# Performance work log

Hardware: AMD Instinct MI355X
Metric: run time of the kernel (lower is better)

## Reference

```python
import jax, jax.numpy as jnp
import numpy as np

B, N, K, S_IN, S_OUT, C, FD = 32, 325, 20, 12, 12, 10, 64
ALPHA = 0.5  # LeakyReLU negative slope

def leaky(x):
    return jnp.where(x >= 0, x, ALPHA * x)

def setup_inputs() -> dict:
    key = jax.random.key(0)
    ks = jax.random.split(key, 9)
    s = 0.2
    return {
        "fushed_features": jax.random.normal(ks[0], (B, N, FD), jnp.float32),
        "input_data": jax.random.normal(ks[1], (B, N, S_IN), jnp.float32),
        "w_W": jax.random.normal(ks[2], (S_IN, S_OUT), jnp.float32) * s,
        "w_b": jax.random.normal(ks[3], (S_OUT,), jnp.float32) * s,
        "a1_W": jax.random.normal(ks[4], (2 * S_OUT, 4 * S_OUT), jnp.float32) * s,
        "a1_b": jax.random.normal(ks[5], (4 * S_OUT,), jnp.float32) * s,
        "a2_W": jax.random.normal(ks[6], (4 * S_OUT, C), jnp.float32) * s,
        "a2_b": jax.random.normal(ks[7], (C,), jnp.float32) * s,
        "adj_mx_topk_index": jax.random.randint(ks[8], (B, N, K), 0, N),
    }

def reference(fushed_features, input_data, w_W, w_b, a1_W, a1_b, a2_W, a2_b, adj_mx_topk_index):
    # w_net: Linear + LeakyReLU -> wh [B,N,S_OUT]
    wh = leaky(input_data @ w_W + w_b)
    # a_net on cat([wh_i, wh_j]): split first linear to avoid materializing [B,N,N,2*S_OUT]
    hx = wh @ a1_W[:S_OUT]   # contribution of wh_x (row node i)
    hy = wh @ a1_W[S_OUT:]   # contribution of wh_y (col node j)
    hidden = leaky(hx[:, :, None, :] + hy[:, None, :, :] + a1_b)   # [B,N,N,4*S_OUT]
    attention = leaky(hidden @ a2_W + a2_b)                        # [B,N,N,C]
    idx = adj_mx_topk_index                                        # [B,N,K]
    # gather top-k neighbors along dim 2
    idx_c = jnp.broadcast_to(idx[..., None], idx.shape + (attention.shape[-1],))
    attention_mask = jnp.take_along_axis(attention, idx_c, axis=2)  # [B,N,K,C]
    attention_mask = jax.nn.softmax(attention_mask, axis=-1)
    # gather neighbor features: wh_expand_top_k[b,i,k] = wh[b, idx[b,i,k]]
    wh_topk = wh[jnp.arange(wh.shape[0])[:, None, None], idx]       # [B,N,K,S_OUT]
    # output = attention_mask^T @ wh_topk
    output_data = jnp.einsum('bnkc,bnks->bncs', attention_mask, wh_topk)
    # clustering loss on detached neighbor features (cosine similarity)
    wt = jax.lax.stop_gradient(wh_topk)
    wtn = wt / (jnp.linalg.norm(wt, axis=-1, keepdims=True) + 1e-8)
    dist_mat = jnp.einsum('bnks,bnls->bnkl', wtn, wtn)              # [B,N,K,K]
    same = (dist_mat >= 0.5).astype(dist_mat.dtype)
    diff = 1.0 - same
    prob = jnp.einsum('bnkc,bnlc->bnkl', attention_mask, attention_mask)
    prob = jnp.clip(prob, 1e-4, 1.0 - 1e-4)
    logp = jnp.log(prob)
    cl = -(same * logp - diff * logp)
    cluster_loss = (cl.sum((-1, -2)) - jnp.trace(cl, axis1=-2, axis2=-1)).mean()
    return output_data, cluster_loss, dist_mat.mean(), wh.mean()
```

## Files before the change

kernel.cpp:

```cpp
#include <hip/hip_runtime.h>
#include <math.h>

#define Bdim 32
#define Ndim 325
#define Kdim 20
#define Sdim 12
#define Cdim 10
#define Hdim 48
#define NB   (Bdim*Ndim)
#define OUT_SCALARS (NB*Cdim*Sdim)
#define BN_BLOCKS (NB/4)
#define NODE_BLOCKS 260
#define NPB 40

#define O_WH  0
#define O_HX  (O_WH + NB*Sdim)
#define O_HY  (O_HX + NB*Hdim)
#define O_PCL (O_HY + NB*Hdim)
#define O_PDS (O_PCL + BN_BLOCKS)
#define O_PWH (O_PDS + BN_BLOCKS)
#define WS_BASE_FLOATS (O_PWH + NODE_BLOCKS)

__device__ __forceinline__ float leaky(float x) { return x >= 0.f ? x : 0.5f * x; }

__global__ __launch_bounds__(256)
void node_kernel(const float* __restrict__ x,
                 const float* __restrict__ wW, const float* __restrict__ wb,
                 const float* __restrict__ A1, const float* __restrict__ b1,
                 float* __restrict__ ws)
{
    __shared__ float s_wh[NPB][Sdim];
    __shared__ float s_r[4];
    const int tid = threadIdx.x;
    const int base = blockIdx.x * NPB;

    float v = 0.f;
    #pragma unroll
    for (int rep = 0; rep < 2; rep++) {
        const int e = tid + rep * 256;
        if (e < NPB * Sdim) {
            const int n = e / Sdim, s = e - n * Sdim;
            const float* xr = x + (size_t)(base + n) * Sdim;
            float acc = wb[s];
            #pragma unroll
            for (int i = 0; i < Sdim; i++) acc += xr[i] * wW[i * Sdim + s];
            acc = leaky(acc);
            s_wh[n][s] = acc;
            ws[O_WH + (size_t)(base + n) * Sdim + s] = acc;
            v += acc;
        }
    }
    __syncthreads();

    #pragma unroll
    for (int rep = 0; rep < 15; rep++) {
        const int e = tid + rep * 256;
        const int n = e / 96, r = e - n * 96;
        const int which = r / Hdim, d = r - which * Hdim;
        const float4 w0 = *(const float4*)&s_wh[n][0];
        const float4 w1 = *(const float4*)&s_wh[n][4];
        const float4 w2 = *(const float4*)&s_wh[n][8];
        const float* Ac = A1 + (which * Sdim) * Hdim + d;
        float acc = which ? 0.f : b1[d];
        acc += w0.x*Ac[0*Hdim] + w0.y*Ac[1*Hdim] + w0.z*Ac[2*Hdim] + w0.w*Ac[3*Hdim]
             + w1.x*Ac[4*Hdim] + w1.y*Ac[5*Hdim] + w1.z*Ac[6*Hdim] + w1.w*Ac[7*Hdim]
             + w2.x*Ac[8*Hdim] + w2.y*Ac[9*Hdim] + w2.z*Ac[10*Hdim] + w2.w*Ac[11*Hdim];
        ws[(which ? O_HY : O_HX) + (size_t)(base + n) * Hdim + d] = acc;
    }

    #pragma unroll
    for (int off = 32; off > 0; off >>= 1) v += __shfl_down(v, off);
    if ((tid & 63) == 0) s_r[tid >> 6] = v;
    __syncthreads();
    if (tid == 0) ws[O_PWH + blockIdx.x] = s_r[0] + s_r[1] + s_r[2] + s_r[3];
}

__device__ __forceinline__ float dot12(const float4& a0, const float4& a1, const float4& a2,
                                       const float4& b0, const float4& b1, const float4& b2)
{
    return a0.x*b0.x + a0.y*b0.y + a0.z*b0.z + a0.w*b0.w
         + a1.x*b1.x + a1.y*b1.y + a1.z*b1.z + a1.w*b1.w
         + a2.x*b2.x + a2.y*b2.y + a2.z*b2.z + a2.w*b2.w;
}

__global__ __launch_bounds__(256)
void mega_kernel(const int* __restrict__ topk,
                 const float* __restrict__ A2, const float* __restrict__ b2,
                 float* __restrict__ ws, float* __restrict__ out)
{
    __shared__ float s_A2  [Hdim * 12];
    __shared__ int   s_topk[80];
    __shared__ float s_whj [4][Kdim][12];
    __shared__ float s_am  [4][Kdim][12];
    __shared__ float s_invn[4][Kdim];
    __shared__ float s_red[2][4];

    const int tid = threadIdx.x;
    const int slot = tid >> 6, t = tid & 63;

    if (tid < 120) {
        const int e0 = tid * 4;
        #pragma unroll
        for (int u = 0; u < 4; u++) {
            const int e = e0 + u;
            const int d = e / Cdim, c = e - d * Cdim;
            s_A2[d * 12 + c] = A2[e];
        }
    } else if (tid < 200) {
        s_topk[tid - 120] = topk[blockIdx.x * 80 + (tid - 120)];
    }
    __syncthreads();

    if (tid < 160) {
        const int e = tid >> 1, half = tid & 1;
        const int gid = blockIdx.x * 80 + e;
        const int bn_e = gid / Kdim;
        const int b_e  = bn_e / Ndim;
        const int j    = s_topk[e];
        const int ek   = e / 20, kk = e - ek * 20;

        const float4* hx4 = (const float4*)(ws + O_HX + (size_t)bn_e * Hdim) + half * 6;
        const float4* hy4 = (const float4*)(ws + O_HY + ((size_t)b_e * Ndim + j) * Hdim) + half * 6;

        float4 xv[6], yv[6];
        #pragma unroll
        for (int q = 0; q < 6; q++) xv[q] = hx4[q];
        #pragma unroll
        for (int q = 0; q < 6; q++) yv[q] = hy4[q];

        float acc[Cdim];
        #pragma unroll
        for (int c = 0; c < Cdim; c++) acc[c] = 0.f;
        #pragma unroll
        for (int q = 0; q < 6; q++) {
            const float hh[4] = { leaky(xv[q].x + yv[q].x), leaky(xv[q].y + yv[q].y),
                                  leaky(xv[q].z + yv[q].z), leaky(xv[q].w + yv[q].w) };
            #pragma unroll
            for (int i = 0; i < 4; i++) {
                const int d = half * 24 + q * 4 + i;
                const float* Ar = &s_A2[d * 12];
                const float4 r0 = *(const float4*)(Ar + 0);
                const float4 r1 = *(const float4*)(Ar + 4);
                const float2 r2 = *(const float2*)(Ar + 8);
                const float h = hh[i];
                acc[0] += h * r0.x; acc[1] += h * r0.y;
                acc[2] += h * r0.z; acc[3] += h * r0.w;
                acc[4] += h * r1.x; acc[5] += h * r1.y;
                acc[6] += h * r1.z; acc[7] += h * r1.w;
                acc[8] += h * r2.x; acc[9] += h * r2.y;
            }
        }
        float full[Cdim];
        #pragma unroll
        for (int c = 0; c < Cdim; c++) full[c] = acc[c] + __shfl_xor(acc[c], 1);
        if (half == 0) {
            float m = -1e30f;
            #pragma unroll
            for (int c = 0; c < Cdim; c++) { full[c] = leaky(full[c] + b2[c]); m = fmaxf(m, full[c]); }
            float sum = 0.f;
            #pragma unroll
            for (int c = 0; c < Cdim; c++) { full[c] = __expf(full[c] - m); sum += full[c]; }
            const float inv = 1.f / sum;
            *(float4*)&s_am[ek][kk][0] = make_float4(full[0]*inv, full[1]*inv, full[2]*inv, full[3]*inv);
            *(float4*)&s_am[ek][kk][4] = make_float4(full[4]*inv, full[5]*inv, full[6]*inv, full[7]*inv);
            *(float4*)&s_am[ek][kk][8] = make_float4(full[8]*inv, full[9]*inv, 0.f, 0.f);
        }
    } else {
        for (int i = tid - 160; i < 240; i += 96) {
            const int kf = i / 3, q = i - kf * 3;
            const int sl = kf / 20, k = kf - sl * 20;
            const int bn_i = (blockIdx.x * 80 + kf) / Kdim;
            const int b_i  = bn_i / Ndim;
            const int j    = s_topk[kf];
            const float4 v = *(const float4*)(ws + O_WH + ((size_t)b_i * Ndim + j) * Sdim + q * 4);
            *(float4*)&s_whj[sl][k][q * 4] = v;
        }
    }
    __syncthreads();

    const int bn = blockIdx.x * 4 + slot;
    float cl = 0.f, ds = 0.f;

    if (t < Kdim) {
        const float4 w0 = *(const float4*)&s_whj[slot][t][0];
        const float4 w1 = *(const float4*)&s_whj[slot][t][4];
        const float4 w2 = *(const float4*)&s_whj[slot][t][8];
        const float nn = dot12(w0, w1, w2, w0, w1, w2);
        const float invn = 1.f / (sqrtf(nn) + 1e-8f);
        s_invn[slot][t] = invn;
        ds += nn * invn * invn;
    } else if (t < Kdim + 30) {
        const int e = t - Kdim, c = e / 3, sq = e - c * 3;
        float4 o = make_float4(0.f, 0.f, 0.f, 0.f);
        #pragma unroll
        for (int k = 0; k < Kdim; k++) {
            const float a = s_am[slot][k][c];
            const float4 w = *(const float4*)&s_whj[slot][k][sq * 4];
            o.x += a * w.x; o.y += a * w.y; o.z += a * w.z; o.w += a * w.w;
        }
        *(float4*)(out + (size_t)bn * (Cdim * Sdim) + c * Sdim + sq * 4) = o;
    }
    __syncthreads();

    if (tid < 220) {
        const int slot_l = tid / 55;
        const int t55 = tid - slot_l * 55;
        const int gi = (int)((21.0f - sqrtf((float)(441 - 8 * t55))) * 0.5f);
        const int gj = gi + (t55 - (gi * (21 - gi)) / 2);
        const int i0 = 2 * gi, j0 = 2 * gj;
        const bool diag = (gi == gj);

        const float4* W = (const float4*)&s_whj[slot_l][0][0];
        const float4* P = (const float4*)&s_am [slot_l][0][0];

        float4 wi[2][3], wj[2][3], pi[2][3], pj[2][3];
        #pragma unroll
        for (int u = 0; u < 2; u++) {
            #pragma unroll
            for (int q = 0; q < 3; q++) {
                wi[u][q] = W[(i0 + u) * 3 + q];
                wj[u][q] = W[(j0 + u) * 3 + q];
                pi[u][q] = P[(i0 + u) * 3 + q];
                pj[u][q] = P[(j0 + u) * 3 + q];
            }
        }
        const float inv_i[2] = { s_invn[slot_l][i0], s_invn[slot_l][i0 + 1] };
        const float inv_j[2] = { s_invn[slot_l][j0], s_invn[slot_l][j0 + 1] };

        #pragma unroll
        for (int ii = 0; ii < 2; ii++) {
            #pragma unroll
            for (int jj = 0; jj < 2; jj++) {
                const float wgt = diag ? ((ii == 0 && jj == 1) ? 2.f : 0.f) : 2.f;
                const float draw = dot12(wi[ii][0], wi[ii][1], wi[ii][2],
                                         wj[jj][0], wj[jj][1], wj[jj][2]);
                const float d = draw * inv_i[ii] * inv_j[jj];
                float p = dot12(pi[ii][0], pi[ii][1], pi[ii][2],
                                pj[jj][0], pj[jj][1], pj[jj][2]);
                p = fminf(fmaxf(p, 1e-4f), 1.f - 1e-4f);
                const float lp = __logf(p);
                ds += wgt * d;
                cl += wgt * ((d >= 0.5f) ? -lp : lp);
            }
        }
    }

    #pragma unroll
    for (int off = 32; off > 0; off >>= 1) {
        cl += __shfl_down(cl, off);
        ds += __shfl_down(ds, off);
    }
    if (t == 0) { s_red[0][slot] = cl; s_red[1][slot] = ds; }
    __syncthreads();
    if (tid == 0) {
        ws[O_PCL + blockIdx.x] = s_red[0][0] + s_red[0][1] + s_red[0][2] + s_red[0][3];
        ws[O_PDS + blockIdx.x] = s_red[1][0] + s_red[1][1] + s_red[1][2] + s_red[1][3];
    }
}

__global__ __launch_bounds__(1024)
void finalize(const float* __restrict__ ws, float* __restrict__ out)
{
    const int t = threadIdx.x;
    float cl = 0.f, ds = 0.f, wm = 0.f;
    for (int i = t; i < BN_BLOCKS; i += 1024) {
        cl += ws[O_PCL + i]; ds += ws[O_PDS + i];
    }
    if (t < NODE_BLOCKS) wm = ws[O_PWH + t];
    #pragma unroll
    for (int off = 32; off > 0; off >>= 1) {
        cl += __shfl_down(cl, off);
        ds += __shfl_down(ds, off);
        wm += __shfl_down(wm, off);
    }
    __shared__ float r[3][16];
    const int w = t >> 6, lane = t & 63;
    if (lane == 0) { r[0][w] = cl; r[1][w] = ds; r[2][w] = wm; }
    __syncthreads();
    if (t == 0) {
        float c = 0.f, d = 0.f, m = 0.f;
        #pragma unroll
        for (int i = 0; i < 16; i++) { c += r[0][i]; d += r[1][i]; m += r[2][i]; }
        out[OUT_SCALARS + 0] = c * (1.f / (float)NB);
        out[OUT_SCALARS + 1] = d * (1.f / ((float)NB * Kdim * Kdim));
        out[OUT_SCALARS + 2] = m * (1.f / ((float)NB * Sdim));
    }
}

__global__ void zero_scalars(float* out) {
    const int t = threadIdx.x;
    if (t < 3) out[OUT_SCALARS + t] = 0.f;
}

__global__ __launch_bounds__(64)
void fused_kernel(const float* __restrict__ input_data,
                  const float* __restrict__ w_W,  const float* __restrict__ w_b,
                  const float* __restrict__ a1_W, const float* __restrict__ a1_b,
                  const float* __restrict__ a2_W, const float* __restrict__ a2_b,
                  const int*   __restrict__ topk,
                  float* __restrict__ out)
{
    __shared__ float s_wW[Sdim * Sdim];
    __shared__ float s_wb[Sdim];
    __shared__ float s_A1[2 * Sdim * Hdim];
    __shared__ float s_b1[Hdim];
    __shared__ float s_A2f[Hdim * Cdim];
    __shared__ float s_b2f[Cdim];
    __shared__ float s_whs[Sdim];
    __shared__ float s_hx[Hdim];
    __shared__ float s_whj[Kdim][Sdim + 1];
    __shared__ float s_hid[Kdim][Hdim + 1];
    __shared__ float s_am [Kdim][Cdim + 1];
    __shared__ float s_wtn[Kdim][Sdim + 1];
    __shared__ int   s_idx[Kdim];

    const int t = threadIdx.x, bn = blockIdx.x, b = bn / Ndim;

    for (int i = t; i < Sdim * Sdim; i += 64)      s_wW[i] = w_W[i];
    if (t < Sdim)                                  s_wb[t] = w_b[t];
    for (int i = t; i < 2 * Sdim * Hdim; i += 64)  s_A1[i] = a1_W[i];
    if (t < Hdim)                                  s_b1[t] = a1_b[t];
    for (int i = t; i < Hdim * Cdim; i += 64)      s_A2f[i] = a2_W[i];
    if (t < Cdim)                                  s_b2f[t] = a2_b[t];
    if (t < Kdim)                                  s_idx[t] = topk[(size_t)bn * Kdim + t];
    __syncthreads();

    const float* xs = input_data + (size_t)bn * Sdim;
    if (t < Sdim) {
        float acc = s_wb[t];
        #pragma unroll
        for (int i = 0; i < Sdim; i++) acc += xs[i] * s_wW[i * Sdim + t];
        s_whs[t] = leaky(acc);
    }
    __syncthreads();

    if (t < Hdim) {
        float acc = 0.f;
        #pragma unroll
        for (int s = 0; s < Sdim; s++) acc += s_whs[s] * s_A1[s * Hdim + t];
        s_hx[t] = acc;
    }
    for (int e = t; e < Kdim * Sdim; e += 64) {
        const int k = e / Sdim, ss = e - k * Sdim;
        const float* xj = input_data + ((size_t)b * Ndim + s_idx[k]) * Sdim;
        float acc = s_wb[ss];
        #pragma unroll
        for (int i = 0; i < Sdim; i++) acc += xj[i] * s_wW[i * Sdim + ss];
        s_whj[k][ss] = leaky(acc);
    }
    __syncthreads();

    for (int e = t; e < Kdim * Hdim; e += 64) {
        const int k = e / Hdim, d = e - k * Hdim;
        float acc = s_hx[d] + s_b1[d];
        #pragma unroll
        for (int s = 0; s < Sdim; s++) acc += s_whj[k][s] * s_A1[(Sdim + s) * Hdim + d];
        s_hid[k][d] = leaky(acc);
    }
    __syncthreads();

    for (int e = t; e < Kdim * Cdim; e += 64) {
        const int k = e / Cdim, c = e - k * Cdim;
        float acc = s_b2f[c];
        #pragma unroll
        for (int d = 0; d < Hdim; d++) acc += s_hid[k][d] * s_A2f[d * Cdim + c];
        s_am[k][c] = leaky(acc);
    }
    __syncthreads();

    if (t < Kdim) {
        float m = -1e30f;
        #pragma unroll
        for (int c = 0; c < Cdim; c++) m = fmaxf(m, s_am[t][c]);
        float ex[Cdim]; float sum = 0.f;
        #pragma unroll
        for (int c = 0; c < Cdim; c++) { ex[c] = expf(s_am[t][c] - m); sum += ex[c]; }
        const float inv = 1.f / sum;
        #pragma unroll
        for (int c = 0; c < Cdim; c++) s_am[t][c] = ex[c] * inv;
        float nn = 0.f;
        #pragma unroll
        for (int s = 0; s < Sdim; s++) nn += s_whj[t][s] * s_whj[t][s];
        const float invn = 1.f / (sqrtf(nn) + 1e-8f);
        #pragma unroll
        for (int s = 0; s < Sdim; s++) s_wtn[t][s] = s_whj[t][s] * invn;
    }
    __syncthreads();

    float* op = out + (size_t)bn * (Cdim * Sdim);
    for (int e = t; e < Cdim * Sdim; e += 64) {
        const int c = e / Sdim, ss = e - c * Sdim;
        float acc = 0.f;
        #pragma unroll
        for (int k = 0; k < Kdim; k++) acc += s_am[k][c] * s_whj[k][ss];
        op[e] = acc;
    }

    float cl = 0.f, ds = 0.f;
    for (int e = t; e < Kdim * Kdim; e += 64) {
        const int k = e / Kdim, l = e - k * Kdim;
        float d = 0.f;
        #pragma unroll
        for (int s = 0; s < Sdim; s++) d += s_wtn[k][s] * s_wtn[l][s];
        ds += d;
        if (k != l) {
            float p = 0.f;
            #pragma unroll
            for (int c = 0; c < Cdim; c++) p += s_am[k][c] * s_am[l][c];
            p = fminf(fmaxf(p, 1e-4f), 1.f - 1e-4f);
            const float lp = logf(p);
            cl += (d >= 0.5f) ? -lp : lp;
        }
    }
    float whl = (t < Sdim) ? s_whs[t] : 0.f;
    #pragma unroll
    for (int off = 32; off > 0; off >>= 1) {
        cl  += __shfl_down(cl,  off);
        ds  += __shfl_down(ds,  off);
        whl += __shfl_down(whl, off);
    }
    if (t == 0) {
        atomicAdd(&out[OUT_SCALARS + 0], cl  * (1.f / (float)NB));
        atomicAdd(&out[OUT_SCALARS + 1], ds  * (1.f / ((float)NB * Kdim * Kdim)));
        atomicAdd(&out[OUT_SCALARS + 2], whl * (1.f / ((float)NB * Sdim)));
    }
}

extern "C" void kernel_launch(void* const* d_in, const int* in_sizes, int n_in,
                              void* d_out, int out_size, void* d_ws, size_t ws_size,
                              hipStream_t stream) {
    (void)in_sizes; (void)n_in; (void)out_size;
    const float* input_data = (const float*)d_in[1];
    const float* w_W  = (const float*)d_in[2];
    const float* w_b  = (const float*)d_in[3];
    const float* a1_W = (const float*)d_in[4];
    const float* a1_b = (const float*)d_in[5];
    const float* a2_W = (const float*)d_in[6];
    const float* a2_b = (const float*)d_in[7];
    const int*   topk = (const int*)d_in[8];
    float* out = (float*)d_out;
    float* ws  = (float*)d_ws;

    if (ws_size >= (size_t)WS_BASE_FLOATS * sizeof(float)) {
        hipLaunchKernelGGL(node_kernel, dim3(NODE_BLOCKS), dim3(256), 0, stream,
                           input_data, w_W, w_b, a1_W, a1_b, ws);
        hipLaunchKernelGGL(mega_kernel, dim3(BN_BLOCKS), dim3(256), 0, stream,
                           topk, a2_W, a2_b, ws, out);
        hipLaunchKernelGGL(finalize, dim3(1), dim3(1024), 0, stream, ws, out);
    } else {
        hipLaunchKernelGGL(zero_scalars, dim3(1), dim3(64), 0, stream, out);
        hipLaunchKernelGGL(fused_kernel, dim3(NB), dim3(64), 0, stream,
                           input_data, w_W, w_b, a1_W, a1_b, a2_W, a2_b, topk, out);
    }
}
```

Before: 104.6 us.

## Shrink node-kernel blocks and overlap mega-kernel gathers with staging

The node kernel now handles 10 nodes per block instead of 40, launching 1040 blocks for more parallelism, and finalize loops over the larger partial-sum array. In the mega kernel the first shared-memory staging barrier is removed: the attention threads read topk and the hx/hy rows straight from global memory into registers, while the other threads load A2 and the gathered wh rows into registers before writing them to shared memory. This shortens the dependent load chain before the first sync, at the cost of more registers held live across the barrier.

```diff
diff --git a/kernel.cpp b/kernel.cpp
--- a/kernel.cpp
+++ b/kernel.cpp
@@ -10,8 +10,8 @@
 #define NB   (Bdim*Ndim)
 #define OUT_SCALARS (NB*Cdim*Sdim)
 #define BN_BLOCKS (NB/4)
-#define NODE_BLOCKS 260
-#define NPB 40
+#define NODE_BLOCKS 1040
+#define NPB 10
 
 #define O_WH  0
 #define O_HX  (O_WH + NB*Sdim)
@@ -35,37 +35,35 @@
     const int base = blockIdx.x * NPB;
 
     float v = 0.f;
+    if (tid < NPB * Sdim) {
+        const int n = tid / Sdim, s = tid - n * Sdim;
+        const float* xr = x + (size_t)(base + n) * Sdim;
+        float acc = wb[s];
+        #pragma unroll
+        for (int i = 0; i < Sdim; i++) acc += xr[i] * wW[i * Sdim + s];
+        acc = leaky(acc);
+        s_wh[n][s] = acc;
+        ws[O_WH + (size_t)(base + n) * Sdim + s] = acc;
+        v += acc;
+    }
+    __syncthreads();
+
     #pragma unroll
-    for (int rep = 0; rep < 2; rep++) {
+    for (int rep = 0; rep < 4; rep++) {
         const int e = tid + rep * 256;
-        if (e < NPB * Sdim) {
-            const int n = e / Sdim, s = e - n * Sdim;
-            const float* xr = x + (size_t)(base + n) * Sdim;
-            float acc = wb[s];
-            #pragma unroll
-            for (int i = 0; i < Sdim; i++) acc += xr[i] * wW[i * Sdim + s];
-            acc = leaky(acc);
-            s_wh[n][s] = acc;
-            ws[O_WH + (size_t)(base + n) * Sdim + s] = acc;
-            v += acc;
-        }
-    }
-    __syncthreads();
-
-    #pragma unroll
-    for (int rep = 0; rep < 15; rep++) {
-        const int e = tid + rep * 256;
-        const int n = e / 96, r = e - n * 96;
-        const int which = r / Hdim, d = r - which * Hdim;
-        const float4 w0 = *(const float4*)&s_wh[n][0];
-        const float4 w1 = *(const float4*)&s_wh[n][4];
-        const float4 w2 = *(const float4*)&s_wh[n][8];
-        const float* Ac = A1 + (which * Sdim) * Hdim + d;
-        float acc = which ? 0.f : b1[d];
-        acc += w0.x*Ac[0*Hdim] + w0.y*Ac[1*Hdim] + w0.z*Ac[2*Hdim] + w0.w*Ac[3*Hdim]
-             + w1.x*Ac[4*Hdim] + w1.y*Ac[5*Hdim] + w1.z*Ac[6*Hdim] + w1.w*Ac[7*Hdim]
-             + w2.x*Ac[8*Hdim] + w2.y*Ac[9*Hdim] + w2.z*Ac[10*Hdim] + w2.w*Ac[11*Hdim];
-        ws[(which ? O_HY : O_HX) + (size_t)(base + n) * Hdim + d] = acc;
+        if (e < NPB * 96) {
+            const int n = e / 96, r = e - n * 96;
+            const int which = r / Hdim, d = r - which * Hdim;
+            const float4 w0 = *(const float4*)&s_wh[n][0];
+            const float4 w1 = *(const float4*)&s_wh[n][4];
+            const float4 w2 = *(const float4*)&s_wh[n][8];
+            const float* Ac = A1 + (which * Sdim) * Hdim + d;
+            float acc = which ? 0.f : b1[d];
+            acc += w0.x*Ac[0*Hdim] + w0.y*Ac[1*Hdim] + w0.z*Ac[2*Hdim] + w0.w*Ac[3*Hdim]
+                 + w1.x*Ac[4*Hdim] + w1.y*Ac[5*Hdim] + w1.z*Ac[6*Hdim] + w1.w*Ac[7*Hdim]
+                 + w2.x*Ac[8*Hdim] + w2.y*Ac[9*Hdim] + w2.z*Ac[10*Hdim] + w2.w*Ac[11*Hdim];
+            ws[(which ? O_HY : O_HX) + (size_t)(base + n) * Hdim + d] = acc;
+        }
     }
 
     #pragma unroll
@@ -89,7 +87,6 @@
                  float* __restrict__ ws, float* __restrict__ out)
 {
     __shared__ float s_A2  [Hdim * 12];
-    __shared__ int   s_topk[80];
     __shared__ float s_whj [4][Kdim][12];
     __shared__ float s_am  [4][Kdim][12];
     __shared__ float s_invn[4][Kdim];
@@ -98,36 +95,69 @@
     const int tid = threadIdx.x;
     const int slot = tid >> 6, t = tid & 63;
 
-    if (tid < 120) {
-        const int e0 = tid * 4;
-        #pragma unroll
-        for (int u = 0; u < 4; u++) {
-            const int e = e0 + u;
-            const int d = e / Cdim, c = e - d * Cdim;
-            s_A2[d * 12 + c] = A2[e];
-        }
-    } else if (tid < 200) {
-        s_topk[tid - 120] = topk[blockIdx.x * 80 + (tid - 120)];
-    }
-    __syncthreads();
+    float4 xv[6], yv[6];
+    int   ek = 0, kk = 0;
 
     if (tid < 160) {
         const int e = tid >> 1, half = tid & 1;
         const int gid = blockIdx.x * 80 + e;
         const int bn_e = gid / Kdim;
         const int b_e  = bn_e / Ndim;
-        const int j    = s_topk[e];
-        const int ek   = e / 20, kk = e - ek * 20;
+        ek = e / 20; kk = e - ek * 20;
 
         const float4* hx4 = (const float4*)(ws + O_HX + (size_t)bn_e * Hdim) + half * 6;
+        #pragma unroll
+        for (int q = 0; q < 6; q++) xv[q] = hx4[q];
+        const int j = topk[gid];
         const float4* hy4 = (const float4*)(ws + O_HY + ((size_t)b_e * Ndim + j) * Hdim) + half * 6;
-
-        float4 xv[6], yv[6];
-        #pragma unroll
-        for (int q = 0; q < 6; q++) xv[q] = hx4[q];
         #pragma unroll
         for (int q = 0; q < 6; q++) yv[q] = hy4[q];
-
+    } else {
+        const int g = tid - 160;
+        float a2v[5];
+        #pragma unroll
+        for (int u = 0; u < 5; u++) a2v[u] = A2[g + u * 96];
+        int   jj[3]; float4 wv[3]; int nt = 0;
+        #pragma unroll
+        for (int u = 0; u < 3; u++) {
+            const int i = g + u * 96;
+            if (i < 240) {
+                const int kf = i / 3;
+                jj[u] = topk[blockIdx.x * 80 + kf];
+                nt++;
+            }
+        }
+        #pragma unroll
+        for (int u = 0; u < 3; u++) {
+            const int i = g + u * 96;
+            if (i < 240) {
+                const int kf = i / 3, q = i - kf * 3;
+                const int bn_i = (blockIdx.x * 80 + kf) / Kdim;
+                const int b_i  = bn_i / Ndim;
+                wv[u] = *(const float4*)(ws + O_WH + ((size_t)b_i * Ndim + jj[u]) * Sdim + q * 4);
+            }
+        }
+        (void)nt;
+        #pragma unroll
+        for (int u = 0; u < 5; u++) {
+            const int e = g + u * 96;
+            const int d = e / Cdim, c = e - d * Cdim;
+            s_A2[d * 12 + c] = a2v[u];
+        }
+        #pragma unroll
+        for (int u = 0; u < 3; u++) {
+            const int i = g + u * 96;
+            if (i < 240) {
+                const int kf = i / 3, q = i - kf * 3;
+                const int sl = kf / 20, k = kf - sl * 20;
+                *(float4*)&s_whj[sl][k][q * 4] = wv[u];
+            }
+        }
+    }
+    __syncthreads();
+
+    if (tid < 160) {
+        const int half = tid & 1;
         float acc[Cdim];
         #pragma unroll
         for (int c = 0; c < Cdim; c++) acc[c] = 0.f;
@@ -165,16 +195,6 @@
             *(float4*)&s_am[ek][kk][4] = make_float4(full[4]*inv, full[5]*inv, full[6]*inv, full[7]*inv);
             *(float4*)&s_am[ek][kk][8] = make_float4(full[8]*inv, full[9]*inv, 0.f, 0.f);
         }
-    } else {
-        for (int i = tid - 160; i < 240; i += 96) {
-            const int kf = i / 3, q = i - kf * 3;
-            const int sl = kf / 20, k = kf - sl * 20;
-            const int bn_i = (blockIdx.x * 80 + kf) / Kdim;
-            const int b_i  = bn_i / Ndim;
-            const int j    = s_topk[kf];
-            const float4 v = *(const float4*)(ws + O_WH + ((size_t)b_i * Ndim + j) * Sdim + q * 4);
-            *(float4*)&s_whj[sl][k][q * 4] = v;
-        }
     }
     __syncthreads();
 
@@ -230,13 +250,13 @@
         #pragma unroll
         for (int ii = 0; ii < 2; ii++) {
             #pragma unroll
-            for (int jj = 0; jj < 2; jj++) {
-                const float wgt = diag ? ((ii == 0 && jj == 1) ? 2.f : 0.f) : 2.f;
+            for (int jj2 = 0; jj2 < 2; jj2++) {
+                const float wgt = diag ? ((ii == 0 && jj2 == 1) ? 2.f : 0.f) : 2.f;
                 const float draw = dot12(wi[ii][0], wi[ii][1], wi[ii][2],
-                                         wj[jj][0], wj[jj][1], wj[jj][2]);
-                const float d = draw * inv_i[ii] * inv_j[jj];
+                                         wj[jj2][0], wj[jj2][1], wj[jj2][2]);
+                const float d = draw * inv_i[ii] * inv_j[jj2];
                 float p = dot12(pi[ii][0], pi[ii][1], pi[ii][2],
-                                pj[jj][0], pj[jj][1], pj[jj][2]);
+                                pj[jj2][0], pj[jj2][1], pj[jj2][2]);
                 p = fminf(fmaxf(p, 1e-4f), 1.f - 1e-4f);
                 const float lp = __logf(p);
                 ds += wgt * d;
@@ -266,7 +286,7 @@
     for (int i = t; i < BN_BLOCKS; i += 1024) {
         cl += ws[O_PCL + i]; ds += ws[O_PDS + i];
     }
-    if (t < NODE_BLOCKS) wm = ws[O_PWH + t];
+    for (int i = t; i < NODE_BLOCKS; i += 1024) wm += ws[O_PWH + i];
     #pragma unroll
     for (int off = 32; off > 0; off >>= 1) {
         cl += __shfl_down(cl, off);
```

New measurement: 110.6 us. 1.06x slower.

## Fuse node projection into mega kernel, recomputing neighbor wh and hy per block

Applied to the files above, without the earlier changes.

Removes the separate node_kernel and its workspace round trip for wh, hx and hy. Each mega_kernel block now recomputes the w_net linear and the a1 projections for its 4 own nodes and 80 gathered neighbors in shared memory. This saves a kernel launch and the global writes and scattered reads of the intermediates. The cost is redundant compute: neighbor projections are recomputed about 20 times each, and the kernel uses more shared memory.

```diff
diff --git a/kernel.cpp b/kernel.cpp
--- a/kernel.cpp
+++ b/kernel.cpp
@@ -10,70 +10,13 @@
 #define NB   (Bdim*Ndim)
 #define OUT_SCALARS (NB*Cdim*Sdim)
 #define BN_BLOCKS (NB/4)
-#define NODE_BLOCKS 260
-#define NPB 40
-
-#define O_WH  0
-#define O_HX  (O_WH + NB*Sdim)
-#define O_HY  (O_HX + NB*Hdim)
-#define O_PCL (O_HY + NB*Hdim)
+
+#define O_PCL 0
 #define O_PDS (O_PCL + BN_BLOCKS)
 #define O_PWH (O_PDS + BN_BLOCKS)
-#define WS_BASE_FLOATS (O_PWH + NODE_BLOCKS)
+#define WS_BASE_FLOATS (O_PWH + BN_BLOCKS)
 
 __device__ __forceinline__ float leaky(float x) { return x >= 0.f ? x : 0.5f * x; }
-
-__global__ __launch_bounds__(256)
-void node_kernel(const float* __restrict__ x,
-                 const float* __restrict__ wW, const float* __restrict__ wb,
-                 const float* __restrict__ A1, const float* __restrict__ b1,
-                 float* __restrict__ ws)
-{
-    __shared__ float s_wh[NPB][Sdim];
-    __shared__ float s_r[4];
-    const int tid = threadIdx.x;
-    const int base = blockIdx.x * NPB;
-
-    float v = 0.f;
-    #pragma unroll
-    for (int rep = 0; rep < 2; rep++) {
-        const int e = tid + rep * 256;
-        if (e < NPB * Sdim) {
-            const int n = e / Sdim, s = e - n * Sdim;
-            const float* xr = x + (size_t)(base + n) * Sdim;
-            float acc = wb[s];
-            #pragma unroll
-            for (int i = 0; i < Sdim; i++) acc += xr[i] * wW[i * Sdim + s];
-            acc = leaky(acc);
-            s_wh[n][s] = acc;
-            ws[O_WH + (size_t)(base + n) * Sdim + s] = acc;
-            v += acc;
-        }
-    }
-    __syncthreads();
-
-    #pragma unroll
-    for (int rep = 0; rep < 15; rep++) {
-        const int e = tid + rep * 256;
-        const int n = e / 96, r = e - n * 96;
-        const int which = r / Hdim, d = r - which * Hdim;
-        const float4 w0 = *(const float4*)&s_wh[n][0];
-        const float4 w1 = *(const float4*)&s_wh[n][4];
-        const float4 w2 = *(const float4*)&s_wh[n][8];
-        const float* Ac = A1 + (which * Sdim) * Hdim + d;
-        float acc = which ? 0.f : b1[d];
-        acc += w0.x*Ac[0*Hdim] + w0.y*Ac[1*Hdim] + w0.z*Ac[2*Hdim] + w0.w*Ac[3*Hdim]
-             + w1.x*Ac[4*Hdim] + w1.y*Ac[5*Hdim] + w1.z*Ac[6*Hdim] + w1.w*Ac[7*Hdim]
-             + w2.x*Ac[8*Hdim] + w2.y*Ac[9*Hdim] + w2.z*Ac[10*Hdim] + w2.w*Ac[11*Hdim];
-        ws[(which ? O_HY : O_HX) + (size_t)(base + n) * Hdim + d] = acc;
-    }
-
-    #pragma unroll
-    for (int off = 32; off > 0; off >>= 1) v += __shfl_down(v, off);
-    if ((tid & 63) == 0) s_r[tid >> 6] = v;
-    __syncthreads();
-    if (tid == 0) ws[O_PWH + blockIdx.x] = s_r[0] + s_r[1] + s_r[2] + s_r[3];
-}
 
 __device__ __forceinline__ float dot12(const float4& a0, const float4& a1, const float4& a2,
                                        const float4& b0, const float4& b1, const float4& b2)
@@ -84,16 +27,21 @@
 }
 
 __global__ __launch_bounds__(256)
-void mega_kernel(const int* __restrict__ topk,
+void mega_kernel(const float* __restrict__ x,
+                 const float* __restrict__ wW, const float* __restrict__ wb,
+                 const float* __restrict__ A1, const float* __restrict__ b1,
                  const float* __restrict__ A2, const float* __restrict__ b2,
+                 const int*   __restrict__ topk,
                  float* __restrict__ ws, float* __restrict__ out)
 {
-    __shared__ float s_A2  [Hdim * 12];
+    __shared__ float s_wh [84][12];
+    __shared__ float s_hy [80][48];
+    __shared__ float s_hx [4][48];
+    __shared__ float s_A2 [Hdim * 12];
+    __shared__ float s_am [4][Kdim][12];
+    __shared__ float s_invn[4][Kdim];
     __shared__ int   s_topk[80];
-    __shared__ float s_whj [4][Kdim][12];
-    __shared__ float s_am  [4][Kdim][12];
-    __shared__ float s_invn[4][Kdim];
-    __shared__ float s_red[2][4];
+    __shared__ float s_red[3][4];
 
     const int tid = threadIdx.x;
     const int slot = tid >> 6, t = tid & 63;
@@ -111,30 +59,66 @@
     }
     __syncthreads();
 
+    float v = 0.f;
+    #pragma unroll
+    for (int rep = 0; rep < 4; rep++) {
+        const int e = tid + rep * 256;
+        if (e < 84 * Sdim) {
+            const int nn = e / Sdim, s = e - nn * Sdim;
+            int g;
+            if (nn < 4) {
+                g = blockIdx.x * 4 + nn;
+            } else {
+                const int ee = nn - 4;
+                const int sl = ee / 20;
+                const int b  = (blockIdx.x * 4 + sl) / Ndim;
+                g = b * Ndim + s_topk[ee];
+            }
+            const float* xr = x + (size_t)g * Sdim;
+            float acc = wb[s];
+            #pragma unroll
+            for (int i = 0; i < Sdim; i++) acc += xr[i] * wW[i * Sdim + s];
+            acc = leaky(acc);
+            s_wh[nn][s] = acc;
+            if (nn < 4) v += acc;
+        }
+    }
+    __syncthreads();
+
+    #pragma unroll
+    for (int rep = 0; rep < 16; rep++) {
+        const int e = tid + rep * 256;
+        if (e < 84 * Hdim) {
+            const int nn = e / Hdim, d = e - nn * Hdim;
+            const float4 w0 = *(const float4*)&s_wh[nn][0];
+            const float4 w1 = *(const float4*)&s_wh[nn][4];
+            const float4 w2 = *(const float4*)&s_wh[nn][8];
+            const bool own = (nn < 4);
+            const float* Ac = A1 + (own ? 0 : Sdim) * Hdim + d;
+            float acc = own ? b1[d] : 0.f;
+            acc += w0.x*Ac[0*Hdim] + w0.y*Ac[1*Hdim] + w0.z*Ac[2*Hdim] + w0.w*Ac[3*Hdim]
+                 + w1.x*Ac[4*Hdim] + w1.y*Ac[5*Hdim] + w1.z*Ac[6*Hdim] + w1.w*Ac[7*Hdim]
+                 + w2.x*Ac[8*Hdim] + w2.y*Ac[9*Hdim] + w2.z*Ac[10*Hdim] + w2.w*Ac[11*Hdim];
+            if (own) s_hx[nn][d] = acc; else s_hy[nn - 4][d] = acc;
+        }
+    }
+    __syncthreads();
+
     if (tid < 160) {
         const int e = tid >> 1, half = tid & 1;
-        const int gid = blockIdx.x * 80 + e;
-        const int bn_e = gid / Kdim;
-        const int b_e  = bn_e / Ndim;
-        const int j    = s_topk[e];
-        const int ek   = e / 20, kk = e - ek * 20;
-
-        const float4* hx4 = (const float4*)(ws + O_HX + (size_t)bn_e * Hdim) + half * 6;
-        const float4* hy4 = (const float4*)(ws + O_HY + ((size_t)b_e * Ndim + j) * Hdim) + half * 6;
-
-        float4 xv[6], yv[6];
-        #pragma unroll
-        for (int q = 0; q < 6; q++) xv[q] = hx4[q];
-        #pragma unroll
-        for (int q = 0; q < 6; q++) yv[q] = hy4[q];
+        const int ek = e / 20, kk = e - ek * 20;
+
+        const float4* hx4 = (const float4*)&s_hx[ek][half * 24];
+        const float4* hy4 = (const float4*)&s_hy[e][half * 24];
 
         float acc[Cdim];
         #pragma unroll
         for (int c = 0; c < Cdim; c++) acc[c] = 0.f;
         #pragma unroll
         for (int q = 0; q < 6; q++) {
-            const float hh[4] = { leaky(xv[q].x + yv[q].x), leaky(xv[q].y + yv[q].y),
-                                  leaky(xv[q].z + yv[q].z), leaky(xv[q].w + yv[q].w) };
+            const float4 xv = hx4[q], yv = hy4[q];
+            const float hh[4] = { leaky(xv.x + yv.x), leaky(xv.y + yv.y),
+                                  leaky(xv.z + yv.z), leaky(xv.w + yv.w) };
             #pragma unroll
             for (int i = 0; i < 4; i++) {
                 const int d = half * 24 + q * 4 + i;
@@ -165,16 +149,6 @@
             *(float4*)&s_am[ek][kk][4] = make_float4(full[4]*inv, full[5]*inv, full[6]*inv, full[7]*inv);
             *(float4*)&s_am[ek][kk][8] = make_float4(full[8]*inv, full[9]*inv, 0.f, 0.f);
         }
-    } else {
-        for (int i = tid - 160; i < 240; i += 96) {
-            const int kf = i / 3, q = i - kf * 3;
-            const int sl = kf / 20, k = kf - sl * 20;
-            const int bn_i = (blockIdx.x * 80 + kf) / Kdim;
-            const int b_i  = bn_i / Ndim;
-            const int j    = s_topk[kf];
-            const float4 v = *(const float4*)(ws + O_WH + ((size_t)b_i * Ndim + j) * Sdim + q * 4);
-            *(float4*)&s_whj[sl][k][q * 4] = v;
-        }
     }
     __syncthreads();
 
@@ -182,9 +156,9 @@
     float cl = 0.f, ds = 0.f;
 
     if (t < Kdim) {
-        const float4 w0 = *(const float4*)&s_whj[slot][t][0];
-        const float4 w1 = *(const float4*)&s_whj[slot][t][4];
-        const float4 w2 = *(const float4*)&s_whj[slot][t][8];
+        const float4 w0 = *(const float4*)&s_wh[4 + slot * 20 + t][0];
+        const float4 w1 = *(const float4*)&s_wh[4 + slot * 20 + t][4];
+        const float4 w2 = *(const float4*)&s_wh[4 + slot * 20 + t][8];
         const float nn = dot12(w0, w1, w2, w0, w1, w2);
         const float invn = 1.f / (sqrtf(nn) + 1e-8f);
         s_invn[slot][t] = invn;
@@ -195,7 +169,7 @@
         #pragma unroll
         for (int k = 0; k < Kdim; k++) {
             const float a = s_am[slot][k][c];
-            const float4 w = *(const float4*)&s_whj[slot][k][sq * 4];
+            const float4 w = *(const float4*)&s_wh[4 + slot * 20 + k][sq * 4];
             o.x += a * w.x; o.y += a * w.y; o.z += a * w.z; o.w += a * w.w;
         }
         *(float4*)(out + (size_t)bn * (Cdim * Sdim) + c * Sdim + sq * 4) = o;
@@ -210,8 +184,8 @@
         const int i0 = 2 * gi, j0 = 2 * gj;
         const bool diag = (gi == gj);
 
-        const float4* W = (const float4*)&s_whj[slot_l][0][0];
-        const float4* P = (const float4*)&s_am [slot_l][0][0];
+        const float4* W = (const float4*)&s_wh[4 + slot_l * 20][0];
+        const float4* P = (const float4*)&s_am[slot_l][0][0];
 
         float4 wi[2][3], wj[2][3], pi[2][3], pj[2][3];
         #pragma unroll
@@ -249,12 +223,14 @@
     for (int off = 32; off > 0; off >>= 1) {
         cl += __shfl_down(cl, off);
         ds += __shfl_down(ds, off);
-    }
-    if (t == 0) { s_red[0][slot] = cl; s_red[1][slot] = ds; }
+        v  += __shfl_down(v,  off);
+    }
+    if (t == 0) { s_red[0][slot] = cl; s_red[1][slot] = ds; s_red[2][slot] = v; }
     __syncthreads();
     if (tid == 0) {
         ws[O_PCL + blockIdx.x] = s_red[0][0] + s_red[0][1] + s_red[0][2] + s_red[0][3];
         ws[O_PDS + blockIdx.x] = s_red[1][0] + s_red[1][1] + s_red[1][2] + s_red[1][3];
+        ws[O_PWH + blockIdx.x] = s_red[2][0] + s_red[2][1] + s_red[2][2] + s_red[2][3];
     }
 }
 
@@ -264,9 +240,10 @@
     const int t = threadIdx.x;
     float cl = 0.f, ds = 0.f, wm = 0.f;
     for (int i = t; i < BN_BLOCKS; i += 1024) {
-        cl += ws[O_PCL + i]; ds += ws[O_PDS + i];
-    }
-    if (t < NODE_BLOCKS) wm = ws[O_PWH + t];
+        cl += ws[O_PCL + i];
+        ds += ws[O_PDS + i];
+        wm += ws[O_PWH + i];
+    }
     #pragma unroll
     for (int off = 32; off > 0; off >>= 1) {
         cl += __shfl_down(cl, off);
@@ -442,10 +419,8 @@
     float* ws  = (float*)d_ws;
 
     if (ws_size >= (size_t)WS_BASE_FLOATS * sizeof(float)) {
-        hipLaunchKernelGGL(node_kernel, dim3(NODE_BLOCKS), dim3(256), 0, stream,
-                           input_data, w_W, w_b, a1_W, a1_b, ws);
         hipLaunchKernelGGL(mega_kernel, dim3(BN_BLOCKS), dim3(256), 0, stream,
-                           topk, a2_W, a2_b, ws, out);
+                           input_data, w_W, w_b, a1_W, a1_b, a2_W, a2_b, topk, ws, out);
         hipLaunchKernelGGL(finalize, dim3(1), dim3(1024), 0, stream, ws, out);
     } else {
         hipLaunchKernelGGL(zero_scalars, dim3(1), dim3(64), 0, stream, out);
```

After: 111.1 us. 1.06x slower.
